# Kernel tuning notes

Measured on AMD Instinct MI355X. Metric: run time of the kernel, lower is better.

## Reference

```python
import jax, jax.numpy as jnp
import numpy as np

N, IN, OUT, T = 65536, 256, 256, 8


def setup_inputs() -> dict:
    key = jax.random.key(0)
    k1, k2, k3, k4 = jax.random.split(key, 4)
    x = jax.random.normal(k1, (N, IN), dtype=jnp.float32)
    types = jax.random.randint(k2, (N,), 0, T, dtype=jnp.int32)
    # xavier_uniform for W: limit = sqrt(6 / (fan_in + fan_out)) with fan computed
    # on the last two dims (out_size, in_size)
    limit = float(np.sqrt(6.0 / (IN + OUT)))
    W = jax.random.uniform(k3, (T, OUT, IN), dtype=jnp.float32, minval=-limit, maxval=limit)
    # original inits b to zeros; use small random values so the bias path is exercised
    b = 0.01 * jax.random.normal(k4, (T, OUT), dtype=jnp.float32)
    return {"x": x, "types": types, "W": W, "b": b}


def reference(x, types, W, b):
    # out[i] = W[types[i]] @ x[i] + b[types[i]]
    # Grouped-GEMM expressed as a loop over the small fixed set of types,
    # avoiding the huge [N, OUT, IN] gather of W[types].
    num_types = W.shape[0]
    out = b[types]  # [N, OUT]
    for t in range(num_types):
        mask = (types == t)[:, None]  # [N, 1]
        out = out + jnp.where(mask, x @ W[t].T, jnp.float32(0.0))
    return out
```

## Files before the change

kernel.cpp:

```cpp
#include <hip/hip_runtime.h>
#include <hip/hip_bf16.h>
#include <stdint.h>


#define NROWS 65536
#define NTYPES 8
#define KDIM 256
#define ODIM 256
#define BM 128
#define BN 128
#define BK 64

typedef __attribute__((ext_vector_type(8))) short short8;
typedef __attribute__((ext_vector_type(4))) float f32x4;

__device__ __forceinline__ unsigned short f2bf(float f) {
    unsigned int u = __float_as_uint(f);
    u += 0x7fffu + ((u >> 16) & 1u);
    return (unsigned short)(u >> 16);
}

__global__ void prep_kernel(const float* __restrict__ W,
                            unsigned short* __restrict__ Wb,
                            int* __restrict__ cnt) {
    if (blockIdx.x == 0 && threadIdx.x < NTYPES) cnt[threadIdx.x] = 0;
    int i = blockIdx.x * 256 + threadIdx.x;
    float4 v = ((const float4*)W)[i];
    ushort4 p;
    p.x = f2bf(v.x); p.y = f2bf(v.y); p.z = f2bf(v.z); p.w = f2bf(v.w);
    ((ushort4*)Wb)[i] = p;
}

__global__ void bucket_kernel(const int* __restrict__ types,
                              int* __restrict__ cnt,
                              int* __restrict__ idx) {
    __shared__ int h[NTYPES];
    __shared__ int base[NTYPES];
    int i = blockIdx.x * 256 + threadIdx.x;
    if (threadIdx.x < NTYPES) h[threadIdx.x] = 0;
    __syncthreads();
    int t = types[i];
    int r = atomicAdd(&h[t], 1);
    __syncthreads();
    if (threadIdx.x < NTYPES)
        base[threadIdx.x] = atomicAdd(&cnt[threadIdx.x], h[threadIdx.x]);
    __syncthreads();
    idx[t * NROWS + base[t] + r] = i;
}

__global__ __launch_bounds__(256, 2)
void gemm_kernel(const float* __restrict__ x,
                 const float* __restrict__ bias,
                 const unsigned short* __restrict__ Wb,
                 const int* __restrict__ cnt,
                 const int* __restrict__ idx,
                 float* __restrict__ out) {
    const int t = blockIdx.z;
    const int count = cnt[t];
    const int m0 = blockIdx.x * BM;
    if (m0 >= count) return;
    const int n0 = blockIdx.y * BN;

    __shared__ int idx_s[BM];
    __shared__ float bias_s[BN];
    __shared__ unsigned short As[BM * BK];
    __shared__ unsigned short Bs[BN * BK];

    const int tid = threadIdx.x;

    if (tid < BM) {
        int m = m0 + tid;
        idx_s[tid] = (m < count) ? idx[t * NROWS + m] : 0;
    } else {
        bias_s[tid - BM] = bias[t * ODIM + n0 + (tid - BM)];
    }
    __syncthreads();

    const int wave = tid >> 6;
    const int lane = tid & 63;
    const int lr = lane & 15;
    const int lq = lane >> 4;
    const int wm = (wave >> 1) * 64;
    const int wn = (wave & 1) * 64;

    f32x4 acc[4][4] = {};

    const int srow = tid >> 4;
    const int sc   = tid & 15;

    char* AsB = (char*)As;
    char* BsB = (char*)Bs;

    for (int k0 = 0; k0 < KDIM; k0 += BK) {
        #pragma unroll
        for (int j = 0; j < 8; ++j) {
            int row = j * 16 + srow;
            const float4 v = *(const float4*)(x + (size_t)idx_s[row] * KDIM + k0 + sc * 4);
            ushort4 p;
            p.x = f2bf(v.x); p.y = f2bf(v.y); p.z = f2bf(v.z); p.w = f2bf(v.w);
            int ch = (sc >> 1) ^ (row & 7);
            *(ushort4*)(AsB + row * 128 + ch * 16 + (sc & 1) * 8) = p;
        }
        #pragma unroll
        for (int it = 0; it < 4; ++it) {
            int dbyte = wave * 4096 + it * 1024;
            int drow  = (dbyte >> 7) + (lane >> 3);
            int schunk = (lane & 7) ^ (lane >> 3);
            const unsigned short* src =
                Wb + (size_t)(t * ODIM + n0 + drow) * KDIM + k0 + schunk * 8;
            __builtin_amdgcn_global_load_lds(
                (const __attribute__((address_space(1))) void*)src,
                (__attribute__((address_space(3))) void*)(BsB + dbyte),
                16, 0, 0);
        }
        __syncthreads();

        #pragma unroll
        for (int kh = 0; kh < 2; ++kh) {
            short8 af[4], bf[4];
            #pragma unroll
            for (int i = 0; i < 4; ++i) {
                int arow = wm + i * 16 + lr;
                int ach = ((kh << 2) + lq) ^ (arow & 7);
                af[i] = *(const short8*)(AsB + arow * 128 + ach * 16);
            }
            #pragma unroll
            for (int i = 0; i < 4; ++i) {
                int brow = wn + i * 16 + lr;
                int bch = ((kh << 2) + lq) ^ (brow & 7);
                bf[i] = *(const short8*)(BsB + brow * 128 + bch * 16);
            }
            #pragma unroll
            for (int i = 0; i < 4; ++i)
                #pragma unroll
                for (int j = 0; j < 4; ++j)
                    acc[i][j] = __builtin_amdgcn_mfma_f32_16x16x32_bf16(
                        af[i], bf[j], acc[i][j], 0, 0, 0);
        }
        __syncthreads();
    }

    #pragma unroll
    for (int i = 0; i < 4; ++i) {
        int lmBase = wm + i * 16 + lq * 4;
        #pragma unroll
        for (int r = 0; r < 4; ++r) {
            int lm = lmBase + r;
            if (m0 + lm < count) {
                size_t orow = (size_t)idx_s[lm] * ODIM;
                #pragma unroll
                for (int j = 0; j < 4; ++j) {
                    int col = wn + j * 16 + lr;
                    out[orow + n0 + col] = acc[i][j][r] + bias_s[col];
                }
            }
        }
    }
}

extern "C" void kernel_launch(void* const* d_in, const int* in_sizes, int n_in,
                              void* d_out, int out_size, void* d_ws, size_t ws_size,
                              hipStream_t stream) {
    const float* x     = (const float*)d_in[0];
    const int*   types = (const int*)d_in[1];
    const float* W     = (const float*)d_in[2];
    const float* b     = (const float*)d_in[3];
    float* out = (float*)d_out;

    char* ws = (char*)d_ws;
    int* cnt = (int*)ws;
    int* idx = (int*)(ws + 1024);
    unsigned short* Wb = (unsigned short*)(ws + 1024 + (size_t)NTYPES * NROWS * sizeof(int));

    prep_kernel<<<512, 256, 0, stream>>>(W, Wb, cnt);
    bucket_kernel<<<NROWS / 256, 256, 0, stream>>>(types, cnt, idx);
    dim3 grid(NROWS / BM, ODIM / BN, NTYPES);
    gemm_kernel<<<grid, 256, 0, stream>>>(x, b, Wb, cnt, idx, out);
}
```

Baseline: 143.3 us.

## Fuse bucketing into per-row-tile GEMM that loops over types locally

Drops the global bucket kernel and the grouped GEMM grid. Each 512-thread block now takes a contiguous 128-row tile of x, loads the whole tile into LDS as bf16, and sorts its rows by type in shared memory. It then runs MFMA per type group, with each wave covering 32 output columns and reading W fragments straight from global/L2. This removes one launch, the global atomics and the scattered gathers of x, and x is read only once. In exchange, tail groups of each type within a tile are padded to 16 rows, and W is re-read per group with no LDS staging.

```diff
diff --git a/kernel.cpp b/kernel.cpp
--- a/kernel.cpp
+++ b/kernel.cpp
@@ -7,9 +7,7 @@
 #define NTYPES 8
 #define KDIM 256
 #define ODIM 256
-#define BM 128
-#define BN 128
-#define BK 64
+#define BR 128
 
 typedef __attribute__((ext_vector_type(8))) short short8;
 typedef __attribute__((ext_vector_type(4))) float f32x4;
@@ -21,137 +19,114 @@
 }
 
 __global__ void prep_kernel(const float* __restrict__ W,
-                            unsigned short* __restrict__ Wb,
-                            int* __restrict__ cnt) {
-    if (blockIdx.x == 0 && threadIdx.x < NTYPES) cnt[threadIdx.x] = 0;
-    int i = blockIdx.x * 256 + threadIdx.x;
-    float4 v = ((const float4*)W)[i];
-    ushort4 p;
-    p.x = f2bf(v.x); p.y = f2bf(v.y); p.z = f2bf(v.z); p.w = f2bf(v.w);
-    ((ushort4*)Wb)[i] = p;
+                            unsigned short* __restrict__ Wb) {
+    #pragma unroll
+    for (int r = 0; r < 2; ++r) {
+        int j = blockIdx.x * 512 + r * 256 + threadIdx.x;
+        float4 v = ((const float4*)W)[j];
+        ushort4 p;
+        p.x = f2bf(v.x); p.y = f2bf(v.y); p.z = f2bf(v.z); p.w = f2bf(v.w);
+        ((ushort4*)Wb)[j] = p;
+    }
 }
 
-__global__ void bucket_kernel(const int* __restrict__ types,
-                              int* __restrict__ cnt,
-                              int* __restrict__ idx) {
-    __shared__ int h[NTYPES];
-    __shared__ int base[NTYPES];
-    int i = blockIdx.x * 256 + threadIdx.x;
-    if (threadIdx.x < NTYPES) h[threadIdx.x] = 0;
-    __syncthreads();
-    int t = types[i];
-    int r = atomicAdd(&h[t], 1);
-    __syncthreads();
-    if (threadIdx.x < NTYPES)
-        base[threadIdx.x] = atomicAdd(&cnt[threadIdx.x], h[threadIdx.x]);
-    __syncthreads();
-    idx[t * NROWS + base[t] + r] = i;
-}
-
-__global__ __launch_bounds__(256, 2)
-void gemm_kernel(const float* __restrict__ x,
-                 const float* __restrict__ bias,
-                 const unsigned short* __restrict__ Wb,
-                 const int* __restrict__ cnt,
-                 const int* __restrict__ idx,
-                 float* __restrict__ out) {
-    const int t = blockIdx.z;
-    const int count = cnt[t];
-    const int m0 = blockIdx.x * BM;
-    if (m0 >= count) return;
-    const int n0 = blockIdx.y * BN;
-
-    __shared__ int idx_s[BM];
-    __shared__ float bias_s[BN];
-    __shared__ unsigned short As[BM * BK];
-    __shared__ unsigned short Bs[BN * BK];
+__global__ __launch_bounds__(512, 4)
+void typed_linear_kernel(const float* __restrict__ x,
+                         const int* __restrict__ types,
+                         const float* __restrict__ bias,
+                         const unsigned short* __restrict__ Wb,
+                         float* __restrict__ out) {
+    __shared__ unsigned short As[BR * KDIM];
+    __shared__ int rlist[BR];
+    __shared__ int tcnt[NTYPES], tstart[NTYPES], tcur[NTYPES];
 
     const int tid = threadIdx.x;
-
-    if (tid < BM) {
-        int m = m0 + tid;
-        idx_s[tid] = (m < count) ? idx[t * NROWS + m] : 0;
-    } else {
-        bias_s[tid - BM] = bias[t * ODIM + n0 + (tid - BM)];
-    }
-    __syncthreads();
-
     const int wave = tid >> 6;
     const int lane = tid & 63;
     const int lr = lane & 15;
     const int lq = lane >> 4;
-    const int wm = (wave >> 1) * 64;
-    const int wn = (wave & 1) * 64;
+    const int wn = wave * 32;
+    const int row0 = blockIdx.x * BR;
+    char* AsB = (char*)As;
 
-    f32x4 acc[4][4] = {};
-
-    const int srow = tid >> 4;
-    const int sc   = tid & 15;
-
-    char* AsB = (char*)As;
-    char* BsB = (char*)Bs;
-
-    for (int k0 = 0; k0 < KDIM; k0 += BK) {
+    if (tid < NTYPES) tcnt[tid] = 0;
+    __syncthreads();
+    int myt = 0;
+    if (tid < BR) {
+        myt = types[row0 + tid];
+        atomicAdd(&tcnt[myt], 1);
+    }
+    __syncthreads();
+    if (tid == 0) {
+        int acc = 0;
         #pragma unroll
-        for (int j = 0; j < 8; ++j) {
-            int row = j * 16 + srow;
-            const float4 v = *(const float4*)(x + (size_t)idx_s[row] * KDIM + k0 + sc * 4);
-            ushort4 p;
-            p.x = f2bf(v.x); p.y = f2bf(v.y); p.z = f2bf(v.z); p.w = f2bf(v.w);
-            int ch = (sc >> 1) ^ (row & 7);
-            *(ushort4*)(AsB + row * 128 + ch * 16 + (sc & 1) * 8) = p;
-        }
-        #pragma unroll
-        for (int it = 0; it < 4; ++it) {
-            int dbyte = wave * 4096 + it * 1024;
-            int drow  = (dbyte >> 7) + (lane >> 3);
-            int schunk = (lane & 7) ^ (lane >> 3);
-            const unsigned short* src =
-                Wb + (size_t)(t * ODIM + n0 + drow) * KDIM + k0 + schunk * 8;
-            __builtin_amdgcn_global_load_lds(
-                (const __attribute__((address_space(1))) void*)src,
-                (__attribute__((address_space(3))) void*)(BsB + dbyte),
-                16, 0, 0);
-        }
-        __syncthreads();
-
-        #pragma unroll
-        for (int kh = 0; kh < 2; ++kh) {
-            short8 af[4], bf[4];
-            #pragma unroll
-            for (int i = 0; i < 4; ++i) {
-                int arow = wm + i * 16 + lr;
-                int ach = ((kh << 2) + lq) ^ (arow & 7);
-                af[i] = *(const short8*)(AsB + arow * 128 + ach * 16);
-            }
-            #pragma unroll
-            for (int i = 0; i < 4; ++i) {
-                int brow = wn + i * 16 + lr;
-                int bch = ((kh << 2) + lq) ^ (brow & 7);
-                bf[i] = *(const short8*)(BsB + brow * 128 + bch * 16);
-            }
-            #pragma unroll
-            for (int i = 0; i < 4; ++i)
-                #pragma unroll
-                for (int j = 0; j < 4; ++j)
-                    acc[i][j] = __builtin_amdgcn_mfma_f32_16x16x32_bf16(
-                        af[i], bf[j], acc[i][j], 0, 0, 0);
-        }
-        __syncthreads();
+        for (int t = 0; t < NTYPES; ++t) { tstart[t] = acc; tcur[t] = acc; acc += tcnt[t]; }
+    }
+    __syncthreads();
+    if (tid < BR) {
+        int p = atomicAdd(&tcur[myt], 1);
+        rlist[p] = tid;
     }
 
+    float breg[NTYPES][2];
     #pragma unroll
-    for (int i = 0; i < 4; ++i) {
-        int lmBase = wm + i * 16 + lq * 4;
+    for (int t = 0; t < NTYPES; ++t)
         #pragma unroll
-        for (int r = 0; r < 4; ++r) {
-            int lm = lmBase + r;
-            if (m0 + lm < count) {
-                size_t orow = (size_t)idx_s[lm] * ODIM;
+        for (int f = 0; f < 2; ++f)
+            breg[t][f] = bias[t * ODIM + wn + f * 16 + lr];
+
+    float4 av[16];
+    const float4* xb = (const float4*)(x + (size_t)row0 * KDIM);
+    #pragma unroll
+    for (int i = 0; i < 16; ++i) av[i] = xb[tid + i * 512];
+    #pragma unroll
+    for (int i = 0; i < 16; ++i) {
+        int flat = tid + i * 512;
+        int row = flat >> 6, c4 = flat & 63;
+        ushort4 p;
+        p.x = f2bf(av[i].x); p.y = f2bf(av[i].y); p.z = f2bf(av[i].z); p.w = f2bf(av[i].w);
+        int ch = (c4 >> 1) ^ (row & 7);
+        *(ushort4*)(AsB + row * 512 + ch * 16 + (c4 & 1) * 8) = p;
+    }
+    __syncthreads();
+
+    const size_t wb_lane = (size_t)(wn + lr) * KDIM + lq * 8;
+    #pragma unroll
+    for (int t = 0; t < NTYPES; ++t) {
+        const int cnt = tcnt[t];
+        if (cnt == 0) continue;
+        const int st = tstart[t];
+        const int ng = (cnt + 15) >> 4;
+        const unsigned short* bt = Wb + (size_t)t * (ODIM * KDIM) + wb_lane;
+        for (int g = 0; g < ng; ++g) {
+            int slotA = g * 16 + lr;
+            int rA = rlist[st + (slotA < cnt ? slotA : cnt - 1)];
+            int abase = rA * 512;
+            int asw = rA & 7;
+
+            short8 bf[2][8];
+            #pragma unroll
+            for (int f = 0; f < 2; ++f)
                 #pragma unroll
-                for (int j = 0; j < 4; ++j) {
-                    int col = wn + j * 16 + lr;
-                    out[orow + n0 + col] = acc[i][j][r] + bias_s[col];
+                for (int kc = 0; kc < 8; ++kc)
+                    bf[f][kc] = *(const short8*)(bt + f * 16 * KDIM + kc * 32);
+
+            f32x4 acc0 = {}, acc1 = {};
+            #pragma unroll
+            for (int kc = 0; kc < 8; ++kc) {
+                short8 af = *(const short8*)(AsB + abase + ((((kc << 2) + lq) ^ asw) << 4));
+                acc0 = __builtin_amdgcn_mfma_f32_16x16x32_bf16(af, bf[0][kc], acc0, 0, 0, 0);
+                acc1 = __builtin_amdgcn_mfma_f32_16x16x32_bf16(af, bf[1][kc], acc1, 0, 0, 0);
+            }
+
+            #pragma unroll
+            for (int r = 0; r < 4; ++r) {
+                int slot = g * 16 + lq * 4 + r;
+                if (slot < cnt) {
+                    int orow = row0 + rlist[st + slot];
+                    float* op = out + (size_t)orow * ODIM + wn;
+                    op[lr]      = acc0[r] + breg[t][0];
+                    op[16 + lr] = acc1[r] + breg[t][1];
                 }
             }
         }
@@ -167,13 +142,8 @@
     const float* b     = (const float*)d_in[3];
     float* out = (float*)d_out;
 
-    char* ws = (char*)d_ws;
-    int* cnt = (int*)ws;
-    int* idx = (int*)(ws + 1024);
-    unsigned short* Wb = (unsigned short*)(ws + 1024 + (size_t)NTYPES * NROWS * sizeof(int));
+    unsigned short* Wb = (unsigned short*)d_ws;
 
-    prep_kernel<<<512, 256, 0, stream>>>(W, Wb, cnt);
-    bucket_kernel<<<NROWS / 256, 256, 0, stream>>>(types, cnt, idx);
-    dim3 grid(NROWS / BM, ODIM / BN, NTYPES);
-    gemm_kernel<<<grid, 256, 0, stream>>>(x, b, Wb, cnt, idx, out);
+    prep_kernel<<<256, 256, 0, stream>>>(W, Wb);
+    typed_linear_kernel<<<NROWS / BR, 512, 0, stream>>>(x, types, b, Wb, out);
 }
```

New measurement: 166.6 us. 16.2% more time.
